# Performance work log

Measured on AMD Instinct MI355X. Metric: run time of the kernel, lower is better.

## Reference

```python
import jax, jax.numpy as jnp
import numpy as np

N = 100000      # nodes
E = 1600000     # edges (avg degree 16)
IN = 128
H = 128
OUT = 64
L = 4


def setup_inputs() -> dict:
    key = jax.random.key(0)
    ks = jax.random.split(key, 12)
    x = jax.random.normal(ks[0], (N, IN), dtype=jnp.float32)
    edge_index = jax.random.randint(ks[1], (2, E), 0, N, dtype=jnp.int64)
    def glorot(k, shp):
        return jax.random.normal(k, shp, dtype=jnp.float32) * (1.0 / np.sqrt(shp[0]))
    inp = {"x": x, "edge_index": edge_index}
    dims = [(IN, H), (H, H), (H, H), (H, H)]
    for i, (fi, fo) in enumerate(dims):
        inp[f"W{i}"] = glorot(ks[2 + i], (fi, fo))
        inp[f"b{i}"] = jnp.zeros((fo,), dtype=jnp.float32)
    inp["lin_W"] = glorot(ks[10], (L * H, OUT))
    inp["lin_b"] = jnp.zeros((OUT,), dtype=jnp.float32)
    return inp


def reference(x, W0, b0, W1, b1, W2, b2, W3, b3, lin_W, lin_b, edge_index):
    # GCN with self-loops and symmetric normalization D^-1/2 (A+I) D^-1/2
    loop = jnp.arange(N, dtype=edge_index.dtype)
    src = jnp.concatenate([edge_index[0], loop])  # [E+N]
    dst = jnp.concatenate([edge_index[1], loop])  # [E+N]
    deg = jax.ops.segment_sum(jnp.ones_like(dst, dtype=x.dtype), dst, N)  # [N]
    dinv = jnp.where(deg > 0, jax.lax.rsqrt(deg), 0.0)
    ew = dinv[src] * dinv[dst]  # per-edge norm [E+N]

    params = [(W0, b0), (W1, b1), (W2, b2), (W3, b3)]
    xs = []
    h = x
    for W, b in params:
        h = h @ W                                            # [N, H]
        msg = h[src] * ew[:, None]                           # gather [E+N, H]
        h = jax.ops.segment_sum(msg, dst, N) + b             # scatter-add [N, H]
        h = jax.nn.relu(h)                                   # dropout p=0 -> identity
        xs.append(h)
    jk = jnp.concatenate(xs, axis=-1)                        # [N, L*H]
    logits = jk @ lin_W + lin_b                              # [N, OUT]
    return jax.nn.log_softmax(logits, axis=-1)
```

## Files before the change

kernel.cpp:

```cpp
#include <hip/hip_runtime.h>
#include <cstdint>
#include <cstddef>

#define NN 100000
#define NE 1600000
#define NTOT (NE + NN)
#define HF 128
#define OF 64
#define SHARD 12500
#define BCHUNK 2048
#define BCAP 210000
#define KB 32

typedef short bfrag_t __attribute__((ext_vector_type(8)));
typedef float f4v     __attribute__((ext_vector_type(4)));


__device__ __forceinline__ unsigned int f2bf_rne(float f) {
    unsigned int u = __float_as_uint(f);
    return (u + 0x7fffu + ((u >> 16) & 1u)) >> 16;
}
__device__ __forceinline__ unsigned int pack_bf2(float lo, float hi) {
    return f2bf_rne(lo) | (f2bf_rne(hi) << 16);
}


__global__ __launch_bounds__(64) void k_init(int* gcnt) {
    if (threadIdx.x < 8) gcnt[threadIdx.x] = 0;
}

__device__ __forceinline__ int nt_load(const int* p) {
    return __builtin_nontemporal_load(p);
}

__global__ __launch_bounds__(256) void k_bin(const int* __restrict__ ei,
                                             int* __restrict__ gcnt,
                                             uint2* __restrict__ binbuf) {
    __shared__ uint2 bins[8][640];
    __shared__ int cnt[8], base[8], anynz;
    int tid = threadIdx.x;
    if (tid < 8) cnt[tid] = 0;
    if (tid == 0) anynz = 0;
    __syncthreads();
    int ebeg = blockIdx.x * BCHUNK;
    int eend = min(NE, ebeg + BCHUNK);
    int v = 0;
    for (int e = ebeg + tid; e < eend; e += 256) v |= nt_load(&ei[2 * e + 1]);
    if (v) anynz = 1;
    __syncthreads();
    bool is64 = (anynz == 0);
    for (int e = ebeg + tid; e < eend; e += 256) {
        int d = is64 ? nt_load(&ei[2 * (NE + e)]) : nt_load(&ei[NE + e]);
        int s = is64 ? nt_load(&ei[2 * e])        : nt_load(&ei[e]);
        int x = (unsigned)d / SHARD;
        int p = atomicAdd(&cnt[x], 1);
        if (p < 640) bins[x][p] = make_uint2((unsigned)d, (unsigned)s);
    }
    __syncthreads();
    if (tid < 8) {
        int c = min(cnt[tid], 640);
        cnt[tid] = c;
        base[tid] = atomicAdd(&gcnt[tid], c);
    }
    __syncthreads();
    for (int x = 0; x < 8; ++x) {
        int c = cnt[x], b0 = base[x];
        for (int i = tid; i < c; i += 256)
            if (b0 + i < BCAP) binbuf[(size_t)x * BCAP + b0 + i] = bins[x][i];
    }
}

__global__ __launch_bounds__(256) void k_cnt(const int* __restrict__ gcnt,
                                             const uint2* __restrict__ binbuf,
                                             int* __restrict__ blockhist) {
    __shared__ int hist[SHARD];
    int tid = threadIdx.x;
    int x = blockIdx.x & 7, kb = blockIdx.x >> 3;
    int n = min(gcnt[x], BCAP);
    int chunk = (n + KB - 1) / KB;
    int beg = kb * chunk, end = min(n, beg + chunk);
    for (int i = tid; i < SHARD; i += 256) hist[i] = 0;
    __syncthreads();
    for (int i = beg + tid; i < end; i += 256) {
        uint2 r = binbuf[(size_t)x * BCAP + i];
        atomicAdd(&hist[r.x - (unsigned)x * SHARD], 1);
    }
    __syncthreads();
    int* bh = blockhist + ((size_t)x * KB + kb) * SHARD;
    for (int i = tid; i < SHARD; i += 256) bh[i] = hist[i];
}

__global__ __launch_bounds__(256) void k_colscan(int* __restrict__ blockhist,
                                                 int* __restrict__ deg) {
    int i = blockIdx.x * 256 + threadIdx.x;
    if (i >= NN) return;
    int x = i / SHARD, ln = i % SHARD;
    int* col = blockhist + (size_t)x * KB * SHARD + ln;
    int s = 0;
#pragma unroll
    for (int kb = 0; kb < KB; ++kb) {
        int c = col[(size_t)kb * SHARD];
        col[(size_t)kb * SHARD] = s;
        s += c;
    }
    deg[i] = 1 + s;
}

__global__ __launch_bounds__(256) void k_scanA(const int* deg, int* rowptr, int* bsum,
                                               float* dinv) {
    __shared__ int sh[256];
    int tid = threadIdx.x;
    int base = blockIdx.x * 1024 + tid * 4;
    int v0 = 0, v1 = 0, v2 = 0, v3 = 0;
    if (base + 0 < NN) v0 = deg[base + 0];
    if (base + 1 < NN) v1 = deg[base + 1];
    if (base + 2 < NN) v2 = deg[base + 2];
    if (base + 3 < NN) v3 = deg[base + 3];
    if (base + 0 < NN) dinv[base + 0] = rsqrtf((float)v0);
    if (base + 1 < NN) dinv[base + 1] = rsqrtf((float)v1);
    if (base + 2 < NN) dinv[base + 2] = rsqrtf((float)v2);
    if (base + 3 < NN) dinv[base + 3] = rsqrtf((float)v3);
    int s = v0 + v1 + v2 + v3;
    sh[tid] = s;
    __syncthreads();
    for (int off = 1; off < 256; off <<= 1) {
        int t = (tid >= off) ? sh[tid - off] : 0;
        __syncthreads();
        sh[tid] += t;
        __syncthreads();
    }
    int run = sh[tid] - s;
    if (base + 0 < NN) rowptr[base + 0] = run; run += v0;
    if (base + 1 < NN) rowptr[base + 1] = run; run += v1;
    if (base + 2 < NN) rowptr[base + 2] = run; run += v2;
    if (base + 3 < NN) rowptr[base + 3] = run;
    if (tid == 255) bsum[blockIdx.x] = sh[255];
}

__global__ __launch_bounds__(128) void k_scanB(const int* bsum, int* boff, int* rowptr) {
    __shared__ int sh[128];
    int tid = threadIdx.x;
    int v = (tid < 98) ? bsum[tid] : 0;
    sh[tid] = v;
    __syncthreads();
    for (int off = 1; off < 128; off <<= 1) {
        int t = (tid >= off) ? sh[tid - off] : 0;
        __syncthreads();
        sh[tid] += t;
        __syncthreads();
    }
    if (tid < 98) boff[tid] = sh[tid] - v;
    if (tid == 0) rowptr[NN] = 0;
}

__global__ __launch_bounds__(256) void k_scanC(int* rowptr, const int* boff, int* csr) {
    int i = blockIdx.x * 256 + threadIdx.x;
    if (i < NN) {
        int r = rowptr[i] + boff[i >> 10];
        rowptr[i] = r;
        csr[r] = i;
        if (i == NN - 1) {  }
    }
    if (blockIdx.x == 0 && threadIdx.x == 0) rowptr[NN] = NTOT;
}

__global__ __launch_bounds__(256) void k_fill(const int* __restrict__ gcnt,
                                              const uint2* __restrict__ binbuf,
                                              const int* __restrict__ blockhist,
                                              const int* __restrict__ rowptr,
                                              int* __restrict__ csr) {
    __shared__ int lrank[SHARD];
    int tid = threadIdx.x;
    int x = blockIdx.x & 7, kb = blockIdx.x >> 3;
    int n = min(gcnt[x], BCAP);
    int chunk = (n + KB - 1) / KB;
    int beg = kb * chunk, end = min(n, beg + chunk);
    for (int i = tid; i < SHARD; i += 256) lrank[i] = 0;
    __syncthreads();
    const int* bh = blockhist + ((size_t)x * KB + kb) * SHARD;
    for (int i = beg + tid; i < end; i += 256) {
        uint2 r = binbuf[(size_t)x * BCAP + i];
        int ln = r.x - (unsigned)x * SHARD;
        int lr = atomicAdd(&lrank[ln], 1);
        csr[rowptr[r.x] + 1 + bh[ln] + lr] = (int)r.y;
    }
}

__global__ __launch_bounds__(256) void k_prep(const float* __restrict__ W0,
                                              const float* __restrict__ W1,
                                              const float* __restrict__ W2,
                                              const float* __restrict__ W3,
                                              const float* __restrict__ linW,
                                              unsigned short* __restrict__ WT,
                                              unsigned short* __restrict__ WjT) {
    int idx = blockIdx.x * 256 + threadIdx.x;
    if (idx < 4 * 128 * 128) {
        int l = idx >> 14, r = idx & 16383, n = r >> 7, k = r & 127;
        const float* Wl = (l == 0) ? W0 : (l == 1) ? W1 : (l == 2) ? W2 : W3;
        WT[idx] = (unsigned short)f2bf_rne(Wl[k * 128 + n]);
    } else if (idx < 4 * 128 * 128 + 4 * 64 * 128) {
        int i2 = idx - 65536;
        int l = i2 >> 13, r = i2 & 8191, n = r >> 7, k = r & 127;
        WjT[i2] = (unsigned short)f2bf_rne(linW[(size_t)(l * 128 + k) * 64 + n]);
    }
}

__global__ __launch_bounds__(256) void k_mmf(const unsigned short* __restrict__ A,
                                             const float* __restrict__ A32,
                                             const unsigned short* __restrict__ WT,
                                             const float* __restrict__ dinv,
                                             unsigned short* __restrict__ m16) {
    __shared__ unsigned short Wlds[128 * 128];
    int tid = threadIdx.x;
    int row0 = blockIdx.x * 64;

    for (int c = tid; c < 2048; c += 256) {
        int row = c >> 4, c16 = c & 15;
        uint4 v = *(const uint4*)&WT[row * 128 + c16 * 8];
        *(uint4*)((char*)Wlds + row * 256 + ((c16 * 16) ^ ((row & 7) << 4))) = v;
    }

    int lane = tid & 63, w = tid >> 6;
    int r15 = lane & 15, q = lane >> 4;
    int xo = (r15 & 7) << 4;

    int arow = row0 + 16 * w + r15;
    bool av = arow < NN;
    bfrag_t afr[4];
#pragma unroll
    for (int ks = 0; ks < 4; ++ks) {
        bfrag_t z = {0, 0, 0, 0, 0, 0, 0, 0};
        if (A32 != nullptr) {
            if (av) {
                float4 u = *(const float4*)&A32[(size_t)arow * 128 + ks * 32 + q * 8];
                float4 v = *(const float4*)&A32[(size_t)arow * 128 + ks * 32 + q * 8 + 4];
                uint4 o;
                o.x = pack_bf2(u.x, u.y);
                o.y = pack_bf2(u.z, u.w);
                o.z = pack_bf2(v.x, v.y);
                o.w = pack_bf2(v.z, v.w);
                afr[ks] = *(bfrag_t*)&o;
            } else afr[ks] = z;
        } else {
            afr[ks] = av ? *(const bfrag_t*)&A[(size_t)arow * 128 + ks * 32 + q * 8] : z;
        }
    }
    __syncthreads();

    f4v acc[8];
#pragma unroll
    for (int i = 0; i < 8; ++i) acc[i] = (f4v){0.f, 0.f, 0.f, 0.f};

#pragma unroll
    for (int ks = 0; ks < 4; ++ks) {
        int ko = ks * 64 + q * 16;
#pragma unroll
        for (int nb = 0; nb < 8; ++nb) {
            bfrag_t b = *(const bfrag_t*)((const char*)Wlds + (nb * 16 + r15) * 256 + (ko ^ xo));
            acc[nb] = __builtin_amdgcn_mfma_f32_16x16x32_bf16(afr[ks], b, acc[nb], 0, 0, 0);
        }
    }

#pragma unroll
    for (int reg = 0; reg < 4; ++reg) {
        int gr = row0 + 16 * w + q * 4 + reg;
        if (gr < NN) {
            float sc = dinv[gr];
#pragma unroll
            for (int nb = 0; nb < 8; ++nb)
                m16[(size_t)gr * 128 + nb * 16 + r15] =
                    (unsigned short)f2bf_rne(acc[nb][reg] * sc);
        }
    }
}

__global__ __launch_bounds__(256) void k_agg(const int* __restrict__ rowptr,
                                             const int* __restrict__ csr,
                                             const uint4* __restrict__ m4,
                                             const float* __restrict__ dinv,
                                             const float* __restrict__ bias,
                                             unsigned short* __restrict__ outb) {
    int w = threadIdx.x >> 6, lane = threadIdx.x & 63;
    int grp = lane >> 4, lj = lane & 15;
    int node = blockIdx.x * 4 + w;
    if (node >= NN) return;
    int beg = rowptr[node], end = rowptr[node + 1];

    float a[8];
#pragma unroll
    for (int q = 0; q < 8; ++q) a[q] = 0.f;

    auto acc8 = [&](uint4 v) {
        a[0] += __uint_as_float(v.x << 16);
        a[1] += __uint_as_float(v.x & 0xffff0000u);
        a[2] += __uint_as_float(v.y << 16);
        a[3] += __uint_as_float(v.y & 0xffff0000u);
        a[4] += __uint_as_float(v.z << 16);
        a[5] += __uint_as_float(v.z & 0xffff0000u);
        a[6] += __uint_as_float(v.w << 16);
        a[7] += __uint_as_float(v.w & 0xffff0000u);
    };

    for (int base = beg; base < end; base += 64) {
        int cnt = min(64, end - base);
        int sv = (lane < cnt) ? csr[base + lane] : 0;
        int k = 0;
        for (; k + 16 <= cnt; k += 16) {
            int s0 = __shfl(sv, k + grp);
            int s1 = __shfl(sv, k + 4 + grp);
            int s2 = __shfl(sv, k + 8 + grp);
            int s3 = __shfl(sv, k + 12 + grp);
            uint4 v0 = m4[(size_t)s0 * 16 + lj];
            uint4 v1 = m4[(size_t)s1 * 16 + lj];
            uint4 v2 = m4[(size_t)s2 * 16 + lj];
            uint4 v3 = m4[(size_t)s3 * 16 + lj];
            acc8(v0); acc8(v1); acc8(v2); acc8(v3);
        }
        for (; k + 4 <= cnt; k += 4) {
            int s = __shfl(sv, k + grp);
            uint4 v = m4[(size_t)s * 16 + lj];
            acc8(v);
        }
        int rem = cnt - k;
        if (rem) {
            int idx = k + grp;
            if (idx >= cnt) idx = cnt - 1;
            int s = __shfl(sv, idx);
            if (grp < rem) {
                uint4 v = m4[(size_t)s * 16 + lj];
                acc8(v);
            }
        }
    }
#pragma unroll
    for (int q = 0; q < 8; ++q) a[q] += __shfl_xor(a[q], 16);
#pragma unroll
    for (int q = 0; q < 8; ++q) a[q] += __shfl_xor(a[q], 32);

    if (grp == 0) {
        float sc = dinv[node];
        float4 b0 = ((const float4*)bias)[lj * 2];
        float4 b1 = ((const float4*)bias)[lj * 2 + 1];
        float r0 = fmaxf(a[0] * sc + b0.x, 0.f);
        float r1 = fmaxf(a[1] * sc + b0.y, 0.f);
        float r2 = fmaxf(a[2] * sc + b0.z, 0.f);
        float r3 = fmaxf(a[3] * sc + b0.w, 0.f);
        float r4 = fmaxf(a[4] * sc + b1.x, 0.f);
        float r5 = fmaxf(a[5] * sc + b1.y, 0.f);
        float r6 = fmaxf(a[6] * sc + b1.z, 0.f);
        float r7 = fmaxf(a[7] * sc + b1.w, 0.f);
        uint4 o;
        o.x = pack_bf2(r0, r1);
        o.y = pack_bf2(r2, r3);
        o.z = pack_bf2(r4, r5);
        o.w = pack_bf2(r6, r7);
        *(uint4*)&outb[(size_t)node * 128 + lj * 8] = o;
    }
}

__global__ __launch_bounds__(256) void k_jk4(const unsigned short* __restrict__ h0,
                                             const unsigned short* __restrict__ h1,
                                             const unsigned short* __restrict__ h2,
                                             const unsigned short* __restrict__ h3,
                                             const unsigned short* __restrict__ WjT,
                                             const float* __restrict__ linb,
                                             float* __restrict__ out) {
    __shared__ unsigned short Wjlds[4 * 64 * 128];
    int tid = threadIdx.x;
    int row0 = blockIdx.x * 64;

    for (int c = tid; c < 4096; c += 256) {
        int row = c >> 4, c16 = c & 15;
        uint4 v = *(const uint4*)&WjT[row * 128 + c16 * 8];
        *(uint4*)((char*)Wjlds + row * 256 + ((c16 * 16) ^ ((row & 7) << 4))) = v;
    }

    int lane = tid & 63, w = tid >> 6;
    int r15 = lane & 15, q = lane >> 4;
    int xo = (r15 & 7) << 4;
    int arow = row0 + 16 * w + r15;
    bool av = arow < NN;
    const unsigned short* hs[4] = {h0, h1, h2, h3};

    __syncthreads();

    f4v accj[4];
#pragma unroll
    for (int i = 0; i < 4; ++i) accj[i] = (f4v){0.f, 0.f, 0.f, 0.f};

#pragma unroll
    for (int l = 0; l < 4; ++l) {
        bfrag_t afr[4];
#pragma unroll
        for (int ks = 0; ks < 4; ++ks) {
            bfrag_t z = {0, 0, 0, 0, 0, 0, 0, 0};
            afr[ks] = av ? *(const bfrag_t*)&hs[l][(size_t)arow * 128 + ks * 32 + q * 8] : z;
        }
#pragma unroll
        for (int ks = 0; ks < 4; ++ks) {
            int ko = ks * 64 + q * 16;
#pragma unroll
            for (int jb = 0; jb < 4; ++jb) {
                bfrag_t b = *(const bfrag_t*)((const char*)Wjlds
                            + (l * 64 + jb * 16 + r15) * 256 + (ko ^ xo));
                accj[jb] = __builtin_amdgcn_mfma_f32_16x16x32_bf16(afr[ks], b, accj[jb], 0, 0, 0);
            }
        }
    }

#pragma unroll
    for (int reg = 0; reg < 4; ++reg) {
        int gr = row0 + 16 * w + q * 4 + reg;
        float v0 = accj[0][reg] + linb[r15];
        float v1 = accj[1][reg] + linb[16 + r15];
        float v2 = accj[2][reg] + linb[32 + r15];
        float v3 = accj[3][reg] + linb[48 + r15];
        float mx = fmaxf(fmaxf(v0, v1), fmaxf(v2, v3));
#pragma unroll
        for (int s = 1; s < 16; s <<= 1) mx = fmaxf(mx, __shfl_xor(mx, s, 16));
        float sum = expf(v0 - mx) + expf(v1 - mx) + expf(v2 - mx) + expf(v3 - mx);
#pragma unroll
        for (int s = 1; s < 16; s <<= 1) sum += __shfl_xor(sum, s, 16);
        float ls = logf(sum) + mx;
        if (gr < NN) {
            out[(size_t)gr * 64 + r15]      = v0 - ls;
            out[(size_t)gr * 64 + 16 + r15] = v1 - ls;
            out[(size_t)gr * 64 + 32 + r15] = v2 - ls;
            out[(size_t)gr * 64 + 48 + r15] = v3 - ls;
        }
    }
}


extern "C" void kernel_launch(void* const* d_in, const int* in_sizes, int n_in,
                              void* d_out, int out_size, void* d_ws, size_t ws_size,
                              hipStream_t stream) {
    const float* x    = (const float*)d_in[0];
    const int*   ei   = (const int*)d_in[1];
    const float* W[4] = {(const float*)d_in[2], (const float*)d_in[4],
                         (const float*)d_in[6], (const float*)d_in[8]};
    const float* b[4] = {(const float*)d_in[3], (const float*)d_in[5],
                         (const float*)d_in[7], (const float*)d_in[9]};
    const float* linW = (const float*)d_in[10];
    const float* linb = (const float*)d_in[11];
    float* out = (float*)d_out;

    char* wp = (char*)d_ws;
    auto alloc = [&](size_t bytes) {
        void* p = (void*)wp;
        wp += (bytes + 255) & ~(size_t)255;
        return p;
    };
    int*   gcnt    = (int*)  alloc(32);
    int*   deg     = (int*)  alloc((size_t)NN * 4);
    float* dinv    = (float*)alloc((size_t)NN * 4);
    int*   rowptr  = (int*)  alloc((size_t)(NN + 1) * 4);
    int*   bsum    = (int*)  alloc(512);
    int*   boff    = (int*)  alloc(512);
    int*   csr     = (int*)  alloc((size_t)NTOT * 4);
    uint2* binbuf  = (uint2*)alloc((size_t)8 * BCAP * 8);
    int*   blockhist = (int*)alloc((size_t)8 * KB * SHARD * 4);
    unsigned short* WT  = (unsigned short*)alloc((size_t)4 * 128 * 128 * 2);
    unsigned short* WjT = (unsigned short*)alloc((size_t)4 * 64 * 128 * 2);
    unsigned short* bufM = (unsigned short*)alloc((size_t)NN * 128 * 2);
    unsigned short* h[4];
    for (int l = 0; l < 4; ++l)
        h[l] = (unsigned short*)alloc((size_t)NN * 128 * 2);

    dim3 blk(256);
    k_init   <<<1, dim3(64), 0, stream>>>(gcnt);
    k_prep   <<<384, blk, 0, stream>>>(W[0], W[1], W[2], W[3], linW, WT, WjT);
    k_bin    <<<(NE + BCHUNK - 1) / BCHUNK, blk, 0, stream>>>(ei, gcnt, binbuf);
    k_cnt    <<<8 * KB, blk, 0, stream>>>(gcnt, binbuf, blockhist);
    k_colscan<<<391, blk, 0, stream>>>(blockhist, deg);
    k_scanA  <<<98, blk, 0, stream>>>(deg, rowptr, bsum, dinv);
    k_scanB  <<<1, dim3(128), 0, stream>>>(bsum, boff, rowptr);
    k_scanC  <<<391, blk, 0, stream>>>(rowptr, boff, csr);
    k_fill   <<<8 * KB, blk, 0, stream>>>(gcnt, binbuf, blockhist, rowptr, csr);

    const unsigned short* lin[4] = {nullptr, h[0], h[1], h[2]};
    for (int l = 0; l < 4; ++l) {
        k_mmf<<<1563, blk, 0, stream>>>(lin[l], l == 0 ? x : nullptr,
                                        WT + (size_t)l * 128 * 128, dinv, bufM);
        k_agg<<<25000, blk, 0, stream>>>(rowptr, csr, (const uint4*)bufM, dinv,
                                         b[l], h[l]);
    }
    k_jk4<<<1563, blk, 0, stream>>>(h[0], h[1], h[2], h[3], WjT, linb, out);
}
```

Measured before the change: 448.5 us.

## Permute feature layout to vectorize matmul stores and simplify aggregation loop

Introduces an interleaved column permutation of hidden features, baked into the transposed bf16 weights. This lets k_mmf write each row's output as one 16-byte store instead of eight scattered 2-byte stores, and the aggregation output keeps the same permuted layout. The input x is converted to bf16 in a separate kernel, so the first matmul uses the same bf16 path. The aggregation loop now loads CSR indices directly per group instead of a wave-wide load plus shuffles. The trade-offs are an extra pass over x, more redundant index loads, and a less unrolled inner loop.

```diff
diff --git a/kernel.cpp b/kernel.cpp
--- a/kernel.cpp
+++ b/kernel.cpp
@@ -11,6 +11,7 @@
 #define BCHUNK 2048
 #define BCAP 210000
 #define KB 32
+
 
 typedef short bfrag_t __attribute__((ext_vector_type(8)));
 typedef float f4v     __attribute__((ext_vector_type(4)));
@@ -150,7 +151,7 @@
         __syncthreads();
     }
     if (tid < 98) boff[tid] = sh[tid] - v;
-    if (tid == 0) rowptr[NN] = 0;
+    if (tid == 0) rowptr[NN] = NTOT;
 }
 
 __global__ __launch_bounds__(256) void k_scanC(int* rowptr, const int* boff, int* csr) {
@@ -159,9 +160,7 @@
         int r = rowptr[i] + boff[i >> 10];
         rowptr[i] = r;
         csr[r] = i;
-        if (i == NN - 1) {  }
-    }
-    if (blockIdx.x == 0 && threadIdx.x == 0) rowptr[NN] = NTOT;
+    }
 }
 
 __global__ __launch_bounds__(256) void k_fill(const int* __restrict__ gcnt,
@@ -184,6 +183,20 @@
         int lr = atomicAdd(&lrank[ln], 1);
         csr[rowptr[r.x] + 1 + bh[ln] + lr] = (int)r.y;
     }
+}
+
+__global__ __launch_bounds__(256) void k_xcvt(const float* __restrict__ x,
+                                              uint4* __restrict__ xb4) {
+    int t = blockIdx.x * 256 + threadIdx.x;
+    if (t >= NN * 16) return;
+    int row = t >> 4, lj = t & 15;
+    const float* xr = x + (size_t)row * 128 + lj;
+    uint4 o;
+    o.x = pack_bf2(xr[0],  xr[16]);
+    o.y = pack_bf2(xr[32], xr[48]);
+    o.z = pack_bf2(xr[64], xr[80]);
+    o.w = pack_bf2(xr[96], xr[112]);
+    xb4[(size_t)row * 16 + lj] = o;
 }
 
 __global__ __launch_bounds__(256) void k_prep(const float* __restrict__ W0,
@@ -195,21 +208,22 @@
                                               unsigned short* __restrict__ WjT) {
     int idx = blockIdx.x * 256 + threadIdx.x;
     if (idx < 4 * 128 * 128) {
-        int l = idx >> 14, r = idx & 16383, n = r >> 7, k = r & 127;
+        int l = idx >> 14, r = idx & 16383, n = r >> 7, p = r & 127;
+        int c = (p & 7) * 16 + (p >> 3);
         const float* Wl = (l == 0) ? W0 : (l == 1) ? W1 : (l == 2) ? W2 : W3;
-        WT[idx] = (unsigned short)f2bf_rne(Wl[k * 128 + n]);
+        WT[idx] = (unsigned short)f2bf_rne(Wl[c * 128 + n]);
     } else if (idx < 4 * 128 * 128 + 4 * 64 * 128) {
         int i2 = idx - 65536;
-        int l = i2 >> 13, r = i2 & 8191, n = r >> 7, k = r & 127;
-        WjT[i2] = (unsigned short)f2bf_rne(linW[(size_t)(l * 128 + k) * 64 + n]);
+        int l = i2 >> 13, r = i2 & 8191, n = r >> 7, p = r & 127;
+        int c = (p & 7) * 16 + (p >> 3);
+        WjT[i2] = (unsigned short)f2bf_rne(linW[(size_t)(l * 128 + c) * 64 + n]);
     }
 }
 
 __global__ __launch_bounds__(256) void k_mmf(const unsigned short* __restrict__ A,
-                                             const float* __restrict__ A32,
                                              const unsigned short* __restrict__ WT,
                                              const float* __restrict__ dinv,
-                                             unsigned short* __restrict__ m16) {
+                                             uint4* __restrict__ m4o) {
     __shared__ unsigned short Wlds[128 * 128];
     int tid = threadIdx.x;
     int row0 = blockIdx.x * 64;
@@ -230,20 +244,7 @@
 #pragma unroll
     for (int ks = 0; ks < 4; ++ks) {
         bfrag_t z = {0, 0, 0, 0, 0, 0, 0, 0};
-        if (A32 != nullptr) {
-            if (av) {
-                float4 u = *(const float4*)&A32[(size_t)arow * 128 + ks * 32 + q * 8];
-                float4 v = *(const float4*)&A32[(size_t)arow * 128 + ks * 32 + q * 8 + 4];
-                uint4 o;
-                o.x = pack_bf2(u.x, u.y);
-                o.y = pack_bf2(u.z, u.w);
-                o.z = pack_bf2(v.x, v.y);
-                o.w = pack_bf2(v.z, v.w);
-                afr[ks] = *(bfrag_t*)&o;
-            } else afr[ks] = z;
-        } else {
-            afr[ks] = av ? *(const bfrag_t*)&A[(size_t)arow * 128 + ks * 32 + q * 8] : z;
-        }
+        afr[ks] = av ? *(const bfrag_t*)&A[(size_t)arow * 128 + ks * 32 + q * 8] : z;
     }
     __syncthreads();
 
@@ -266,10 +267,12 @@
         int gr = row0 + 16 * w + q * 4 + reg;
         if (gr < NN) {
             float sc = dinv[gr];
-#pragma unroll
-            for (int nb = 0; nb < 8; ++nb)
-                m16[(size_t)gr * 128 + nb * 16 + r15] =
-                    (unsigned short)f2bf_rne(acc[nb][reg] * sc);
+            uint4 o;
+            o.x = pack_bf2(acc[0][reg] * sc, acc[1][reg] * sc);
+            o.y = pack_bf2(acc[2][reg] * sc, acc[3][reg] * sc);
+            o.z = pack_bf2(acc[4][reg] * sc, acc[5][reg] * sc);
+            o.w = pack_bf2(acc[6][reg] * sc, acc[7][reg] * sc);
+            m4o[(size_t)gr * 16 + r15] = o;
         }
     }
 }
@@ -279,7 +282,7 @@
                                              const uint4* __restrict__ m4,
                                              const float* __restrict__ dinv,
                                              const float* __restrict__ bias,
-                                             unsigned short* __restrict__ outb) {
+                                             uint4* __restrict__ outb) {
     int w = threadIdx.x >> 6, lane = threadIdx.x & 63;
     int grp = lane >> 4, lj = lane & 15;
     int node = blockIdx.x * 4 + w;
@@ -301,36 +304,16 @@
         a[7] += __uint_as_float(v.w & 0xffff0000u);
     };
 
-    for (int base = beg; base < end; base += 64) {
-        int cnt = min(64, end - base);
-        int sv = (lane < cnt) ? csr[base + lane] : 0;
-        int k = 0;
-        for (; k + 16 <= cnt; k += 16) {
-            int s0 = __shfl(sv, k + grp);
-            int s1 = __shfl(sv, k + 4 + grp);
-            int s2 = __shfl(sv, k + 8 + grp);
-            int s3 = __shfl(sv, k + 12 + grp);
-            uint4 v0 = m4[(size_t)s0 * 16 + lj];
-            uint4 v1 = m4[(size_t)s1 * 16 + lj];
-            uint4 v2 = m4[(size_t)s2 * 16 + lj];
-            uint4 v3 = m4[(size_t)s3 * 16 + lj];
-            acc8(v0); acc8(v1); acc8(v2); acc8(v3);
-        }
-        for (; k + 4 <= cnt; k += 4) {
-            int s = __shfl(sv, k + grp);
-            uint4 v = m4[(size_t)s * 16 + lj];
-            acc8(v);
-        }
-        int rem = cnt - k;
-        if (rem) {
-            int idx = k + grp;
-            if (idx >= cnt) idx = cnt - 1;
-            int s = __shfl(sv, idx);
-            if (grp < rem) {
-                uint4 v = m4[(size_t)s * 16 + lj];
-                acc8(v);
-            }
-        }
+    for (int e = beg; e < end; e += 16) {
+        int e0 = e + grp, e1 = e0 + 4, e2 = e0 + 8, e3 = e0 + 12;
+        int s0 = (e0 < end) ? csr[e0] : 0;
+        int s1 = (e1 < end) ? csr[e1] : 0;
+        int s2 = (e2 < end) ? csr[e2] : 0;
+        int s3 = (e3 < end) ? csr[e3] : 0;
+        if (e0 < end) acc8(m4[(size_t)s0 * 16 + lj]);
+        if (e1 < end) acc8(m4[(size_t)s1 * 16 + lj]);
+        if (e2 < end) acc8(m4[(size_t)s2 * 16 + lj]);
+        if (e3 < end) acc8(m4[(size_t)s3 * 16 + lj]);
     }
 #pragma unroll
     for (int q = 0; q < 8; ++q) a[q] += __shfl_xor(a[q], 16);
@@ -339,22 +322,16 @@
 
     if (grp == 0) {
         float sc = dinv[node];
-        float4 b0 = ((const float4*)bias)[lj * 2];
-        float4 b1 = ((const float4*)bias)[lj * 2 + 1];
-        float r0 = fmaxf(a[0] * sc + b0.x, 0.f);
-        float r1 = fmaxf(a[1] * sc + b0.y, 0.f);
-        float r2 = fmaxf(a[2] * sc + b0.z, 0.f);
-        float r3 = fmaxf(a[3] * sc + b0.w, 0.f);
-        float r4 = fmaxf(a[4] * sc + b1.x, 0.f);
-        float r5 = fmaxf(a[5] * sc + b1.y, 0.f);
-        float r6 = fmaxf(a[6] * sc + b1.z, 0.f);
-        float r7 = fmaxf(a[7] * sc + b1.w, 0.f);
+        float r[8];
+#pragma unroll
+        for (int q = 0; q < 8; ++q)
+            r[q] = fmaxf(a[q] * sc + bias[q * 16 + lj], 0.f);
         uint4 o;
-        o.x = pack_bf2(r0, r1);
-        o.y = pack_bf2(r2, r3);
-        o.z = pack_bf2(r4, r5);
-        o.w = pack_bf2(r6, r7);
-        *(uint4*)&outb[(size_t)node * 128 + lj * 8] = o;
+        o.x = pack_bf2(r[0], r[1]);
+        o.y = pack_bf2(r[2], r[3]);
+        o.z = pack_bf2(r[4], r[5]);
+        o.w = pack_bf2(r[6], r[7]);
+        outb[(size_t)node * 16 + lj] = o;
     }
 }
 
@@ -462,6 +439,7 @@
     int*   blockhist = (int*)alloc((size_t)8 * KB * SHARD * 4);
     unsigned short* WT  = (unsigned short*)alloc((size_t)4 * 128 * 128 * 2);
     unsigned short* WjT = (unsigned short*)alloc((size_t)4 * 64 * 128 * 2);
+    unsigned short* xb   = (unsigned short*)alloc((size_t)NN * 128 * 2);
     unsigned short* bufM = (unsigned short*)alloc((size_t)NN * 128 * 2);
     unsigned short* h[4];
     for (int l = 0; l < 4; ++l)
@@ -470,6 +448,7 @@
     dim3 blk(256);
     k_init   <<<1, dim3(64), 0, stream>>>(gcnt);
     k_prep   <<<384, blk, 0, stream>>>(W[0], W[1], W[2], W[3], linW, WT, WjT);
+    k_xcvt   <<<6250, blk, 0, stream>>>(x, (uint4*)xb);
     k_bin    <<<(NE + BCHUNK - 1) / BCHUNK, blk, 0, stream>>>(ei, gcnt, binbuf);
     k_cnt    <<<8 * KB, blk, 0, stream>>>(gcnt, binbuf, blockhist);
     k_colscan<<<391, blk, 0, stream>>>(blockhist, deg);
@@ -478,12 +457,12 @@
     k_scanC  <<<391, blk, 0, stream>>>(rowptr, boff, csr);
     k_fill   <<<8 * KB, blk, 0, stream>>>(gcnt, binbuf, blockhist, rowptr, csr);
 
-    const unsigned short* lin[4] = {nullptr, h[0], h[1], h[2]};
+    const unsigned short* lin[4] = {xb, h[0], h[1], h[2]};
     for (int l = 0; l < 4; ++l) {
-        k_mmf<<<1563, blk, 0, stream>>>(lin[l], l == 0 ? x : nullptr,
-                                        WT + (size_t)l * 128 * 128, dinv, bufM);
+        k_mmf<<<1563, blk, 0, stream>>>(lin[l], WT + (size_t)l * 128 * 128, dinv,
+                                        (uint4*)bufM);
         k_agg<<<25000, blk, 0, stream>>>(rowptr, csr, (const uint4*)bufM, dinv,
-                                         b[l], h[l]);
+                                         b[l], (uint4*)h[l]);
     }
     k_jk4<<<1563, blk, 0, stream>>>(h[0], h[1], h[2], h[3], WjT, linb, out);
 }
```

New measurement: 502.8 us. 12.1% more time.
